# Performance work log

Measured on AMD Instinct MI355X. Metric: run time of the kernel, lower is better.

Reference implementation:

```python
import jax, jax.numpy as jnp
import numpy as np

B_GRAPHS = 64
N_PER = 8192
N = B_GRAPHS * N_PER          # 524288 nodes
E = N * 24                    # 12582912 edges
F0 = 8                        # num_node_features
FE = 4                        # num_edge_features
HID = 5                       # embedding_size, heads=1
ACT = 4                       # num_actions
GOAL = 6                      # goal_size
EPS = 1e-5


def _graph_norm(x, batch, w, b, ms):
    # PyG GraphNorm: per-graph mean/var with learnable mean_scale
    cnt = jax.ops.segment_sum(jnp.ones((x.shape[0],), x.dtype), batch, num_segments=B_GRAPHS)[:, None]
    mean = jax.ops.segment_sum(x, batch, num_segments=B_GRAPHS) / cnt
    sub = x - ms * mean[batch]
    var = jax.ops.segment_sum(sub * sub, batch, num_segments=B_GRAPHS) / cnt
    return w * sub * jax.lax.rsqrt(var[batch] + EPS) + b


def _gatv2(x, edge_index, edge_attr, Wl, bl, Wr, br, We, att, bo):
    # GATv2Conv, heads=1, add_self_loops=True (self-loop edge_attr = mean of edge_attr)
    n = x.shape[0]
    loop = jnp.arange(n, dtype=edge_index.dtype)
    src = jnp.concatenate([edge_index[0], loop])
    dst = jnp.concatenate([edge_index[1], loop])
    ea = jnp.concatenate([edge_attr, jnp.broadcast_to(edge_attr.mean(0), (n, edge_attr.shape[1]))], axis=0)
    xl = x @ Wl + bl            # source transform [n, HID]
    xr = x @ Wr + br            # target transform [n, HID]
    xl_src = xl[src]            # [E+n, HID]
    e = jax.nn.leaky_relu(xl_src + xr[dst] + ea @ We, 0.2)
    logits = e @ att            # [E+n]
    m = jax.ops.segment_max(logits, dst, num_segments=n)
    ex = jnp.exp(logits - m[dst])
    alpha = ex / jax.ops.segment_sum(ex, dst, num_segments=n)[dst]
    return jax.ops.segment_sum(alpha[:, None] * xl_src, dst, num_segments=n) + bo


def reference(x, edge_index, edge_attr, batch, current_node_ids, action_mask, one_hot_goal,
              gn_w, gn_b, gn_ms,
              Wl1, bl1, Wr1, br1, We1, att1, bo1,
              Wl2, bl2, Wr2, br2, We2, att2, bo2,
              Wv1, bv1, Wv2, bv2, Wa1, ba1, Wa2, ba2):
    x = _graph_norm(x, batch, gn_w, gn_b, gn_ms)
    identity = x
    h = jax.nn.relu(_gatv2(x, edge_index, edge_attr, Wl1, bl1, Wr1, br1, We1, att1, bo1))
    x = jnp.concatenate([h, identity], axis=1)    # [N, 13]
    identity = x
    h = jax.nn.relu(_gatv2(x, edge_index, edge_attr, Wl2, bl2, Wr2, br2, We2, att2, bo2))
    x = jnp.concatenate([h, identity], axis=1)    # [N, 18]
    cnt = jnp.bincount(batch, length=B_GRAPHS)
    pool = jax.ops.segment_sum(x, batch, num_segments=B_GRAPHS) / cnt[:, None].astype(x.dtype)
    offsets = jnp.concatenate([jnp.zeros((1,), cnt.dtype), jnp.cumsum(cnt)[:-1]])
    xg = x[current_node_ids + offsets]            # [B, 18]
    feat = jnp.concatenate([xg, pool, one_hot_goal], axis=1)  # [B, 42]
    adv = jax.nn.relu(feat @ Wa1 + ba1) @ Wa2 + ba2
    val = jax.nn.relu(feat @ Wv1 + bv1) @ Wv2 + bv2
    q = val + adv - adv.mean(axis=1, keepdims=True)
    return jnp.where(action_mask == 0, jnp.asarray(-1e8, q.dtype), q)


def setup_inputs():
    key = jax.random.key(0)
    k = jax.random.split(key, 24)
    lin_w = lambda kk, i, o: (jax.random.normal(kk, (i, o), jnp.float32) / np.sqrt(i)).astype(jnp.float32)
    x = jax.random.normal(k[0], (N, F0), jnp.float32)
    g = jax.random.randint(k[1], (E,), 0, B_GRAPHS)
    src = g * N_PER + jax.random.randint(k[2], (E,), 0, N_PER)
    dst = g * N_PER + jax.random.randint(k[3], (E,), 0, N_PER)
    edge_index = jnp.stack([src, dst]).astype(jnp.int32)
    edge_attr = jax.random.normal(k[4], (E, FE), jnp.float32)
    batch = (jnp.arange(N) // N_PER).astype(jnp.int32)
    current_node_ids = jax.random.randint(k[5], (B_GRAPHS,), 0, N_PER).astype(jnp.int32)
    action_mask = jax.random.randint(k[6], (B_GRAPHS, ACT), 0, 2).astype(jnp.int32)
    one_hot_goal = jax.nn.one_hot(jax.random.randint(k[7], (B_GRAPHS,), 0, GOAL), GOAL, dtype=jnp.float32)
    inp = dict(x=x, edge_index=edge_index, edge_attr=edge_attr, batch=batch,
               current_node_ids=current_node_ids, action_mask=action_mask, one_hot_goal=one_hot_goal)
    inp.update(gn_w=jnp.ones((F0,)), gn_b=jnp.zeros((F0,)), gn_ms=jnp.ones((F0,)))
    inp.update(Wl1=lin_w(k[8], F0, HID), bl1=jnp.zeros((HID,)), Wr1=lin_w(k[9], F0, HID), br1=jnp.zeros((HID,)),
               We1=lin_w(k[10], FE, HID), att1=jax.random.normal(k[11], (HID,), jnp.float32), bo1=jnp.zeros((HID,)))
    inp.update(Wl2=lin_w(k[12], 13, HID), bl2=jnp.zeros((HID,)), Wr2=lin_w(k[13], 13, HID), br2=jnp.zeros((HID,)),
               We2=lin_w(k[14], FE, HID), att2=jax.random.normal(k[15], (HID,), jnp.float32), bo2=jnp.zeros((HID,)))
    inp.update(Wv1=lin_w(k[16], 42, 10), bv1=jnp.zeros((10,)), Wv2=lin_w(k[17], 10, 1), bv2=jnp.zeros((1,)),
               Wa1=lin_w(k[18], 42, 10), ba1=jnp.zeros((10,)), Wa2=lin_w(k[19], 10, ACT), ba2=jnp.zeros((ACT,)))
    return inp
```

## Files before the change

### kernel.cpp

```cpp
#include <hip/hip_runtime.h>
#include <hip/hip_bf16.h>
#include <stdint.h>

#define NG   64
#define NPER 8192
#define NN   (NG * NPER)
#define NE   (NN * 24)
#define F0   8

#define NBIN   1024
#define BROWS  512
#define BCAP   13312
#define SCHUNK 8192
#define NBLK   (NE / SCHUNK)

__device__ __forceinline__ void atomAddF(float* p, float v) {
    unsafeAtomicAdd(p, v);
}

__device__ __forceinline__ uint32_t pk_bf16(float a, float b) {
    return (__float_as_uint(a) >> 16) | (__float_as_uint(b) & 0xFFFF0000u);
}
__device__ __forceinline__ float lo_bf16(uint32_t u) { return __uint_as_float(u << 16); }
__device__ __forceinline__ float hi_bf16(uint32_t u) { return __uint_as_float(u & 0xFFFF0000u); }

__global__ void k_stats(const float* __restrict__ x, float* __restrict__ stats) {
    int b = blockIdx.x;
    int g = b >> 2;
    int seg = b & 3;
    int t = threadIdx.x;
    float sum[8] = {0,0,0,0,0,0,0,0};
    float sq[8]  = {0,0,0,0,0,0,0,0};
    int base = g * NPER + seg * 2048;
    for (int r = t; r < 2048; r += 256) {
        const float4* row = (const float4*)(x + (size_t)(base + r) * F0);
        float4 ra = row[0], rb = row[1];
        float v0=ra.x,v1=ra.y,v2=ra.z,v3=ra.w,v4=rb.x,v5=rb.y,v6=rb.z,v7=rb.w;
        sum[0]+=v0; sq[0]+=v0*v0; sum[1]+=v1; sq[1]+=v1*v1;
        sum[2]+=v2; sq[2]+=v2*v2; sum[3]+=v3; sq[3]+=v3*v3;
        sum[4]+=v4; sq[4]+=v4*v4; sum[5]+=v5; sq[5]+=v5*v5;
        sum[6]+=v6; sq[6]+=v6*v6; sum[7]+=v7; sq[7]+=v7*v7;
    }
    #pragma unroll
    for (int f = 0; f < 8; f++) {
        float s = sum[f], q = sq[f];
        for (int off = 32; off > 0; off >>= 1) {
            s += __shfl_down(s, off);
            q += __shfl_down(q, off);
        }
        if ((t & 63) == 0) {
            atomAddF(stats + g*16 + f, s);
            atomAddF(stats + g*16 + 8 + f, q);
        }
    }
}

__global__ void k_norm(const float* __restrict__ x, const float* __restrict__ stats,
                       const float* __restrict__ gw, const float* __restrict__ gb,
                       const float* __restrict__ gms,
                       const float* __restrict__ Wl, const float* __restrict__ bl,
                       const float* __restrict__ Wr, const float* __restrict__ br,
                       float* __restrict__ xn, uint4* __restrict__ xlc,
                       float* __restrict__ xr1) {
    int g = blockIdx.x >> 5;
    int n = blockIdx.x * 256 + threadIdx.x;
    const float invc = 1.0f / (float)NPER;
    float xnf[8];
    const float4* row4 = (const float4*)(x + (size_t)n * F0);
    float4 ra = row4[0], rb = row4[1];
    float rv[8] = {ra.x, ra.y, ra.z, ra.w, rb.x, rb.y, rb.z, rb.w};
    #pragma unroll
    for (int f = 0; f < 8; f++) {
        float m   = stats[g*16 + f] * invc;
        float ex2 = stats[g*16 + 8 + f] * invc;
        float ms  = gms[f];
        float var = ex2 - 2.0f*ms*m*m + ms*ms*m*m;
        float sub = rv[f] - ms * m;
        xnf[f] = gw[f] * sub * rsqrtf(var + 1e-5f) + gb[f];
    }
    float4* xnr = (float4*)(xn + (size_t)n * 8);
    xnr[0] = make_float4(xnf[0], xnf[1], xnf[2], xnf[3]);
    xnr[1] = make_float4(xnf[4], xnf[5], xnf[6], xnf[7]);
    float xlv[5], xrv[5];
    #pragma unroll
    for (int j = 0; j < 5; j++) {
        float a = bl[j], b = br[j];
        #pragma unroll
        for (int f = 0; f < 8; f++) { a += xnf[f] * Wl[f*5 + j]; b += xnf[f] * Wr[f*5 + j]; }
        xlv[j] = a; xrv[j] = b;
    }
    uint4 p;
    p.x = pk_bf16(xlv[0], xlv[1]);
    p.y = pk_bf16(xlv[2], xlv[3]);
    p.z = pk_bf16(xlv[4], 0.0f);
    p.w = 0u;
    xlc[n] = p;
    float4* xrr = (float4*)(xr1 + (size_t)n * 8);
    xrr[0] = make_float4(xrv[0], xrv[1], xrv[2], xrv[3]);
    xrr[1] = make_float4(xrv[4], 0.f, 0.f, 0.f);
}

__global__ __launch_bounds__(1024) void k_bin(
        const int* __restrict__ src, const int* __restrict__ dst,
        const float4* __restrict__ eattr,
        unsigned* __restrict__ gfill, uint2* __restrict__ payload,
        float* __restrict__ easum) {
    __shared__ unsigned lc[NBIN];
    __shared__ unsigned lstart[NBIN];
    __shared__ unsigned lalloc[NBIN];
    __shared__ unsigned lbase[NBIN];
    __shared__ uint2 stage[SCHUNK];
    __shared__ float ls[16][4];
    __shared__ unsigned wsum[16];
    int t = threadIdx.x;
    int lane = t & 63, wv = t >> 6;
    int base = blockIdx.x * SCHUNK;
    lc[t] = 0u;
    __syncthreads();
    int dc[SCHUNK/1024];
    #pragma unroll
    for (int k = 0; k < SCHUNK/1024; k++) dc[k] = dst[base + k*1024 + t];
    #pragma unroll
    for (int k = 0; k < SCHUNK/1024; k++)
        atomicAdd(&lc[((unsigned)dc[k]) >> 9], 1u);
    __syncthreads();
    unsigned c = lc[t];
    unsigned s = c;
    #pragma unroll
    for (int d = 1; d < 64; d <<= 1) {
        unsigned u = (unsigned)__shfl_up((int)s, d);
        if (lane >= d) s += u;
    }
    if (lane == 63) wsum[wv] = s;
    __syncthreads();
    if (t < 16) {
        unsigned v = wsum[t], sv = v;
        #pragma unroll
        for (int d = 1; d < 16; d <<= 1) {
            unsigned u = (unsigned)__shfl_up((int)sv, d);
            if (t >= d) sv += u;
        }
        wsum[t] = sv - v;
    }
    __syncthreads();
    unsigned excl = s + wsum[wv] - c;
    lstart[t] = excl;
    lalloc[t] = excl;
    lbase[t]  = c ? atomicAdd(&gfill[t], c) : 0u;
    __syncthreads();
    float e0 = 0.f, e1 = 0.f, e2 = 0.f, e3 = 0.f;
    unsigned xwv[SCHUNK/1024], ywv[SCHUNK/1024], bv[SCHUNK/1024], pos[SCHUNK/1024];
    #pragma unroll
    for (int k = 0; k < SCHUNK/1024; k++) {
        int e = base + k*1024 + t;
        int sv2 = src[e];
        int d = dc[k];
        float4 ea = eattr[e];
        e0 += ea.x; e1 += ea.y; e2 += ea.z; e3 += ea.w;
        bv[k] = ((unsigned)d) >> 9;
        xwv[k] = (unsigned)(sv2 & 8191) | ((unsigned)(d & 511) << 13) | (bv[k] << 22);
        ywv[k] = __builtin_amdgcn_cvt_pk_fp8_f32(ea.z, ea.w,
                    __builtin_amdgcn_cvt_pk_fp8_f32(ea.x, ea.y, 0, false), true);
    }
    #pragma unroll
    for (int k = 0; k < SCHUNK/1024; k++) pos[k] = atomicAdd(&lalloc[bv[k]], 1u);
    #pragma unroll
    for (int k = 0; k < SCHUNK/1024; k++) stage[pos[k]] = make_uint2(xwv[k], ywv[k]);
    __syncthreads();
    for (int i = t; i < SCHUNK; i += 1024) {
        uint2 r = stage[i];
        unsigned b = r.x >> 22;
        unsigned loc = lbase[b] + ((unsigned)i - lstart[b]);
        if (loc < BCAP) payload[(size_t)b * BCAP + loc] = r;
    }
    for (int off = 32; off > 0; off >>= 1) {
        e0 += __shfl_down(e0, off); e1 += __shfl_down(e1, off);
        e2 += __shfl_down(e2, off); e3 += __shfl_down(e3, off);
    }
    if ((t & 63) == 0) { ls[wv][0]=e0; ls[wv][1]=e1; ls[wv][2]=e2; ls[wv][3]=e3; }
    __syncthreads();
    if (t < 4) {
        float v = 0.f;
        #pragma unroll
        for (int k = 0; k < 16; k++) v += ls[k][t];
        atomAddF(easum + t, v);
    }
}

template<int PASS>
__global__ __launch_bounds__(1024) void k_edge(
        const uint2* __restrict__ payload, const unsigned* __restrict__ gfill,
        const uint4* __restrict__ xlcv, const float* __restrict__ xrf,
        const float* __restrict__ xn, const float* __restrict__ h1in,
        const float* __restrict__ We, const float* __restrict__ att,
        const float* __restrict__ bo, const float* __restrict__ easum,
        const float* __restrict__ Wl2, const float* __restrict__ bl2,
        const float* __restrict__ Wr2, const float* __restrict__ br2,
        float* __restrict__ h1out, uint4* __restrict__ xl2c, float* __restrict__ xr2,
        const int* __restrict__ cur, float* __restrict__ pool, float* __restrict__ xg) {
    __shared__ uint2 stage[BCAP + 6];
    __shared__ unsigned cnt_s[BROWS];
    __shared__ unsigned scan_s[BROWS];
    __shared__ unsigned alloc_s[BROWS];
    __shared__ unsigned wscan[8];
    __shared__ float lsum[16][18];
    int t = threadIdx.x;
    int lane = t & 63, wvi = t >> 6;
    int bin = ((blockIdx.x & 7) << 7) + (blockIdx.x >> 3);
    int g = bin >> 4;

    unsigned CNT = gfill[bin];
    if (CNT > BCAP) CNT = BCAP;
    const uint2* pA = payload + (size_t)bin * BCAP;

    uint2 rcv[13];
    #pragma unroll
    for (int k = 0; k < 13; ++k) {
        unsigned idx = (unsigned)(k * 1024) + (unsigned)t;
        rcv[k] = (idx < CNT) ? pA[idx] : make_uint2(0u, 0u);
    }
    if (t < BROWS) cnt_s[t] = 0u;
    __syncthreads();
    #pragma unroll
    for (int k = 0; k < 13; ++k) {
        unsigned idx = (unsigned)(k * 1024) + (unsigned)t;
        if (idx < CNT) atomicAdd(&cnt_s[(rcv[k].x >> 13) & 511u], 1u);
    }
    __syncthreads();
    unsigned c = 0, s = 0;
    if (t < BROWS) {
        c = cnt_s[t];
        s = c;
        #pragma unroll
        for (int d = 1; d < 64; d <<= 1) {
            unsigned u = (unsigned)__shfl_up((int)s, d);
            if (lane >= d) s += u;
        }
        if (lane == 63) wscan[wvi] = s;
    }
    __syncthreads();
    if (t < 8) {
        unsigned v = wscan[t], sv = v;
        #pragma unroll
        for (int d = 1; d < 8; d <<= 1) {
            unsigned u = (unsigned)__shfl_up((int)sv, d);
            if (t >= d) sv += u;
        }
        wscan[t] = sv - v;
    }
    __syncthreads();
    if (t < BROWS) {
        unsigned incl = s + wscan[wvi];
        scan_s[t]  = incl;
        alloc_s[t] = incl - c;
    }
    __syncthreads();
    unsigned pos[13];
    #pragma unroll
    for (int k = 0; k < 13; ++k) {
        unsigned idx = (unsigned)(k * 1024) + (unsigned)t;
        pos[k] = (idx < CNT) ? atomicAdd(&alloc_s[(rcv[k].x >> 13) & 511u], 1u) : 0u;
    }
    #pragma unroll
    for (int k = 0; k < 13; ++k) {
        unsigned idx = (unsigned)(k * 1024) + (unsigned)t;
        if (idx < CNT) stage[pos[k]] = rcv[k];
    }
    __syncthreads();

    int r = t >> 1, sub = t & 1;
    int n = (bin << 9) + r;
    unsigned end   = scan_s[r];
    unsigned start = end - cnt_s[r];

    float w0[5], w1[5], w2[5], w3[5], av[5];
    #pragma unroll
    for (int j = 0; j < 5; j++) {
        w0[j] = We[j]; w1[j] = We[5+j]; w2[j] = We[10+j]; w3[j] = We[15+j];
        av[j] = att[j];
    }
    const uint4* xlg = xlcv + ((size_t)g << 13);
    const float4* xr4 = (const float4*)(xrf + (size_t)n * 8);
    float4 q0 = xr4[0], q1 = xr4[1];
    float xrv[5] = {q0.x, q0.y, q0.z, q0.w, q1.x};

    float acc[5] = {0.f, 0.f, 0.f, 0.f, 0.f};
    float aw = 0.f;

    unsigned i0 = start + (unsigned)sub;
    uint2 r0 = stage[i0];
    uint4 x0 = xlg[r0.x & 8191u];
    uint2 r1 = stage[i0 + 2];
    uint4 x1 = xlg[r1.x & 8191u];
    for (unsigned i = i0; i < end; i += 2) {
        uint2 rn = stage[i + 4];
        uint4 xf = xlg[rn.x & 8191u];
        float xs[5] = {lo_bf16(x0.x), hi_bf16(x0.x),
                       lo_bf16(x0.y), hi_bf16(x0.y), lo_bf16(x0.z)};
        float eax = __builtin_amdgcn_cvt_f32_fp8(r0.y, 0);
        float eay = __builtin_amdgcn_cvt_f32_fp8(r0.y, 1);
        float eaz = __builtin_amdgcn_cvt_f32_fp8(r0.y, 2);
        float eaw = __builtin_amdgcn_cvt_f32_fp8(r0.y, 3);
        float lg = 0.f;
        #pragma unroll
        for (int j = 0; j < 5; j++) {
            float z = xs[j] + xrv[j] + w0[j]*eax + w1[j]*eay + w2[j]*eaz + w3[j]*eaw;
            z = z > 0.f ? z : 0.2f * z;
            lg += z * av[j];
        }
        float w = __expf(lg);
        aw += w;
        #pragma unroll
        for (int j = 0; j < 5; j++) acc[j] += w * xs[j];
        r0 = r1; x0 = x1; r1 = rn; x1 = xf;
    }
    aw += __shfl_xor(aw, 1);
    #pragma unroll
    for (int j = 0; j < 5; j++) acc[j] += __shfl_xor(acc[j], 1);

    const float invE = 1.0f / (float)NE;
    float eaM[5];
    #pragma unroll
    for (int j = 0; j < 5; j++)
        eaM[j] = (easum[0]*w0[j] + easum[1]*w1[j] + easum[2]*w2[j] + easum[3]*w3[j]) * invE;
    uint4 xw = xlcv[n];
    float xlv[5] = {lo_bf16(xw.x), hi_bf16(xw.x),
                    lo_bf16(xw.y), hi_bf16(xw.y), lo_bf16(xw.z)};
    float lg = 0.f;
    #pragma unroll
    for (int j = 0; j < 5; j++) {
        float z = xlv[j] + xrv[j] + eaM[j];
        z = z > 0.f ? z : 0.2f * z;
        lg += z * av[j];
    }
    float wsl = __expf(lg);
    float den = aw + wsl;
    float h[5];
    #pragma unroll
    for (int j = 0; j < 5; j++) {
        float v = (acc[j] + wsl * xlv[j]) / den + bo[j];
        h[j] = v > 0.f ? v : 0.f;
    }
    const float4* xnr = (const float4*)(xn + (size_t)n * 8);
    float4 xa = xnr[0], xb = xnr[1];

    if (PASS == 1) {
        float x2[13];
        #pragma unroll
        for (int j = 0; j < 5; j++) x2[j] = h[j];
        x2[5] = xa.x; x2[6] = xa.y; x2[7] = xa.z; x2[8] = xa.w;
        x2[9] = xb.x; x2[10] = xb.y; x2[11] = xb.z; x2[12] = xb.w;
        const float* Wx = sub ? Wr2 : Wl2;
        const float* bx = sub ? br2 : bl2;
        float o[5];
        #pragma unroll
        for (int j = 0; j < 5; j++) {
            float a = bx[j];
            #pragma unroll
            for (int k = 0; k < 13; k++) a += x2[k] * Wx[k*5 + j];
            o[j] = a;
        }
        if (sub) {
            float4* xr2r = (float4*)(xr2 + (size_t)n * 8);
            xr2r[0] = make_float4(o[0], o[1], o[2], o[3]);
            xr2r[1] = make_float4(o[4], 0.f, 0.f, 0.f);
            float4* h1r = (float4*)(h1out + (size_t)n * 8);
            h1r[0] = make_float4(h[0], h[1], h[2], h[3]);
            (h1out + (size_t)n * 8)[4] = h[4];
        } else {
            uint4 p;
            p.x = pk_bf16(o[0], o[1]);
            p.y = pk_bf16(o[2], o[3]);
            p.z = pk_bf16(o[4], 0.0f);
            p.w = 0u;
            xl2c[n] = p;
        }
    } else {
        float x3[18];
        #pragma unroll
        for (int j = 0; j < 5; j++) x3[j] = h[j];
        const float* h1r = h1in + (size_t)n * 8;
        #pragma unroll
        for (int j = 0; j < 5; j++) x3[5 + j] = h1r[j];
        x3[10] = xa.x; x3[11] = xa.y; x3[12] = xa.z; x3[13] = xa.w;
        x3[14] = xb.x; x3[15] = xb.y; x3[16] = xb.z; x3[17] = xb.w;
        #pragma unroll
        for (int f = 0; f < 18; f++) {
            float v = sub ? 0.f : x3[f];
            for (int off = 32; off > 0; off >>= 1) v += __shfl_down(v, off);
            if ((t & 63) == 0) lsum[wvi][f] = v;
        }
        __syncthreads();
        if (t < 18) {
            float v = 0.f;
            #pragma unroll
            for (int k = 0; k < 16; k++) v += lsum[k][t];
            atomAddF(pool + g*18 + t, v);
        }
        if (!sub && ((n & (NPER - 1)) == cur[g])) {
            #pragma unroll
            for (int f = 0; f < 18; f++) xg[g*18 + f] = x3[f];
        }
    }
}

__global__ void k_head(const float* __restrict__ xg, const float* __restrict__ pool,
                       const float* __restrict__ goal, const int* __restrict__ am,
                       const float* __restrict__ Wv1, const float* __restrict__ bv1,
                       const float* __restrict__ Wv2, const float* __restrict__ bv2,
                       const float* __restrict__ Wa1, const float* __restrict__ ba1,
                       const float* __restrict__ Wa2, const float* __restrict__ ba2,
                       float* __restrict__ out) {
    int g = threadIdx.x;
    if (g >= NG) return;
    float feat[42];
    #pragma unroll
    for (int f = 0; f < 18; f++) feat[f] = xg[g*18 + f];
    #pragma unroll
    for (int f = 0; f < 18; f++) feat[18 + f] = pool[g*18 + f] * (1.0f / (float)NPER);
    #pragma unroll
    for (int f = 0; f < 6; f++) feat[36 + f] = goal[g*6 + f];
    float hv[10], ha[10];
    #pragma unroll
    for (int j = 0; j < 10; j++) {
        float a = bv1[j], b = ba1[j];
        for (int k = 0; k < 42; k++) { a += feat[k] * Wv1[k*10 + j]; b += feat[k] * Wa1[k*10 + j]; }
        hv[j] = a > 0.f ? a : 0.f;
        ha[j] = b > 0.f ? b : 0.f;
    }
    float val = bv2[0];
    #pragma unroll
    for (int k = 0; k < 10; k++) val += hv[k] * Wv2[k];
    float adv[4];
    #pragma unroll
    for (int a2 = 0; a2 < 4; a2++) {
        float s = ba2[a2];
        #pragma unroll
        for (int k = 0; k < 10; k++) s += ha[k] * Wa2[k*4 + a2];
        adv[a2] = s;
    }
    float mean = 0.25f * (adv[0] + adv[1] + adv[2] + adv[3]);
    #pragma unroll
    for (int a2 = 0; a2 < 4; a2++) {
        float q = val + adv[a2] - mean;
        if (am[g*4 + a2] == 0) q = -1e8f;
        out[g*4 + a2] = q;
    }
}

extern "C" void kernel_launch(void* const* d_in, const int* in_sizes, int n_in,
                              void* d_out, int out_size, void* d_ws, size_t ws_size,
                              hipStream_t stream) {
    const float* x     = (const float*)d_in[0];
    const int*   ei    = (const int*)  d_in[1];
    const float* eattr = (const float*)d_in[2];
    const int*   cur   = (const int*)  d_in[4];
    const int*   am    = (const int*)  d_in[5];
    const float* goal  = (const float*)d_in[6];
    const float* gw    = (const float*)d_in[7];
    const float* gb    = (const float*)d_in[8];
    const float* gms   = (const float*)d_in[9];
    const float* Wl1   = (const float*)d_in[10];
    const float* bl1   = (const float*)d_in[11];
    const float* Wr1   = (const float*)d_in[12];
    const float* br1   = (const float*)d_in[13];
    const float* We1   = (const float*)d_in[14];
    const float* att1  = (const float*)d_in[15];
    const float* bo1   = (const float*)d_in[16];
    const float* Wl2   = (const float*)d_in[17];
    const float* bl2   = (const float*)d_in[18];
    const float* Wr2   = (const float*)d_in[19];
    const float* br2   = (const float*)d_in[20];
    const float* We2   = (const float*)d_in[21];
    const float* att2  = (const float*)d_in[22];
    const float* bo2   = (const float*)d_in[23];
    const float* Wv1   = (const float*)d_in[24];
    const float* bv1   = (const float*)d_in[25];
    const float* Wv2   = (const float*)d_in[26];
    const float* bv2   = (const float*)d_in[27];
    const float* Wa1   = (const float*)d_in[28];
    const float* ba1   = (const float*)d_in[29];
    const float* Wa2   = (const float*)d_in[30];
    const float* ba2   = (const float*)d_in[31];

    float* ws   = (float*)d_ws;
    float* xn   = ws;
    float* xr1  = xn  + (size_t)NN * 8;
    float* xr2  = xr1 + (size_t)NN * 8;
    float* h1   = xr2 + (size_t)NN * 8;
    uint4* xlc  = (uint4*)(h1 + (size_t)NN * 8);
    uint4* xl2c = xlc + (size_t)NN;
    uint2* payload = (uint2*)(xl2c + (size_t)NN);
    unsigned* gfill = (unsigned*)(payload + (size_t)NBIN * BCAP + 8);
    float* stats = (float*)(gfill + NBIN);
    float* easum = stats + NG * 16;
    float* pool  = easum + 4;
    float* xg    = pool + NG * 18;

    size_t zbytes = (size_t)(NBIN + NG*16 + 4 + NG*18) * 4;
    hipMemsetAsync(gfill, 0, zbytes, stream);

    k_stats<<<256, 256, 0, stream>>>(x, stats);
    k_norm<<<NN/256, 256, 0, stream>>>(x, stats, gw, gb, gms, Wl1, bl1, Wr1, br1,
                                       xn, xlc, xr1);
    k_bin<<<NBLK, 1024, 0, stream>>>(ei, ei + NE, (const float4*)eattr,
                                     gfill, payload, easum);
    k_edge<1><<<NBIN, 1024, 0, stream>>>(payload, gfill, xlc, xr1, xn, nullptr,
                                         We1, att1, bo1, easum,
                                         Wl2, bl2, Wr2, br2,
                                         h1, xl2c, xr2,
                                         nullptr, nullptr, nullptr);
    k_edge<2><<<NBIN, 1024, 0, stream>>>(payload, gfill, xl2c, xr2, xn, h1,
                                         We2, att2, bo2, easum,
                                         nullptr, nullptr, nullptr, nullptr,
                                         nullptr, nullptr, nullptr,
                                         cur, pool, xg);
    k_head<<<1, 64, 0, stream>>>(xg, pool, goal, am, Wv1, bv1, Wv2, bv2,
                                 Wa1, ba1, Wa2, ba2, (float*)d_out);
}
```

Measured before the change: 681.2 us.

## Process edge bins in two LDS halves to raise occupancy

```diff
diff --git a/kernel.cpp b/kernel.cpp
--- a/kernel.cpp
+++ b/kernel.cpp
@@ -11,6 +11,7 @@
 #define NBIN   1024
 #define BROWS  512
 #define BCAP   13312
+#define SHALF  6656
 #define SCHUNK 8192
 #define NBLK   (NE / SCHUNK)
 
@@ -100,15 +101,13 @@
     xrr[1] = make_float4(xrv[4], 0.f, 0.f, 0.f);
 }
 
-__global__ __launch_bounds__(1024) void k_bin(
+__global__ __launch_bounds__(1024, 8) void k_bin(
         const int* __restrict__ src, const int* __restrict__ dst,
         const float4* __restrict__ eattr,
         unsigned* __restrict__ gfill, uint2* __restrict__ payload,
         float* __restrict__ easum) {
     __shared__ unsigned lc[NBIN];
-    __shared__ unsigned lstart[NBIN];
-    __shared__ unsigned lalloc[NBIN];
-    __shared__ unsigned lbase[NBIN];
+    __shared__ unsigned diff[NBIN];
     __shared__ uint2 stage[SCHUNK];
     __shared__ float ls[16][4];
     __shared__ unsigned wsum[16];
@@ -144,9 +143,9 @@
     }
     __syncthreads();
     unsigned excl = s + wsum[wv] - c;
-    lstart[t] = excl;
-    lalloc[t] = excl;
-    lbase[t]  = c ? atomicAdd(&gfill[t], c) : 0u;
+    unsigned gbase = c ? atomicAdd(&gfill[t], c) : 0u;
+    lc[t]   = excl;
+    diff[t] = gbase - excl;
     __syncthreads();
     float e0 = 0.f, e1 = 0.f, e2 = 0.f, e3 = 0.f;
     unsigned xwv[SCHUNK/1024], ywv[SCHUNK/1024], bv[SCHUNK/1024], pos[SCHUNK/1024];
@@ -163,14 +162,14 @@
                     __builtin_amdgcn_cvt_pk_fp8_f32(ea.x, ea.y, 0, false), true);
     }
     #pragma unroll
-    for (int k = 0; k < SCHUNK/1024; k++) pos[k] = atomicAdd(&lalloc[bv[k]], 1u);
+    for (int k = 0; k < SCHUNK/1024; k++) pos[k] = atomicAdd(&lc[bv[k]], 1u);
     #pragma unroll
     for (int k = 0; k < SCHUNK/1024; k++) stage[pos[k]] = make_uint2(xwv[k], ywv[k]);
     __syncthreads();
     for (int i = t; i < SCHUNK; i += 1024) {
         uint2 r = stage[i];
         unsigned b = r.x >> 22;
-        unsigned loc = lbase[b] + ((unsigned)i - lstart[b]);
+        unsigned loc = (unsigned)i + diff[b];
         if (loc < BCAP) payload[(size_t)b * BCAP + loc] = r;
     }
     for (int off = 32; off > 0; off >>= 1) {
@@ -188,7 +187,7 @@
 }
 
 template<int PASS>
-__global__ __launch_bounds__(1024) void k_edge(
+__global__ __launch_bounds__(1024, 8) void k_edge(
         const uint2* __restrict__ payload, const unsigned* __restrict__ gfill,
         const uint4* __restrict__ xlcv, const float* __restrict__ xrf,
         const float* __restrict__ xn, const float* __restrict__ h1in,
@@ -198,7 +197,7 @@
         const float* __restrict__ Wr2, const float* __restrict__ br2,
         float* __restrict__ h1out, uint4* __restrict__ xl2c, float* __restrict__ xr2,
         const int* __restrict__ cur, float* __restrict__ pool, float* __restrict__ xg) {
-    __shared__ uint2 stage[BCAP + 6];
+    __shared__ uint2 stage[SHALF + 8];
     __shared__ unsigned cnt_s[BROWS];
     __shared__ unsigned scan_s[BROWS];
     __shared__ unsigned alloc_s[BROWS];
@@ -213,72 +212,14 @@
     if (CNT > BCAP) CNT = BCAP;
     const uint2* pA = payload + (size_t)bin * BCAP;
 
-    uint2 rcv[13];
-    #pragma unroll
-    for (int k = 0; k < 13; ++k) {
-        unsigned idx = (unsigned)(k * 1024) + (unsigned)t;
-        rcv[k] = (idx < CNT) ? pA[idx] : make_uint2(0u, 0u);
-    }
-    if (t < BROWS) cnt_s[t] = 0u;
-    __syncthreads();
-    #pragma unroll
-    for (int k = 0; k < 13; ++k) {
-        unsigned idx = (unsigned)(k * 1024) + (unsigned)t;
-        if (idx < CNT) atomicAdd(&cnt_s[(rcv[k].x >> 13) & 511u], 1u);
-    }
-    __syncthreads();
-    unsigned c = 0, s = 0;
-    if (t < BROWS) {
-        c = cnt_s[t];
-        s = c;
-        #pragma unroll
-        for (int d = 1; d < 64; d <<= 1) {
-            unsigned u = (unsigned)__shfl_up((int)s, d);
-            if (lane >= d) s += u;
-        }
-        if (lane == 63) wscan[wvi] = s;
-    }
-    __syncthreads();
-    if (t < 8) {
-        unsigned v = wscan[t], sv = v;
-        #pragma unroll
-        for (int d = 1; d < 8; d <<= 1) {
-            unsigned u = (unsigned)__shfl_up((int)sv, d);
-            if (t >= d) sv += u;
-        }
-        wscan[t] = sv - v;
-    }
-    __syncthreads();
-    if (t < BROWS) {
-        unsigned incl = s + wscan[wvi];
-        scan_s[t]  = incl;
-        alloc_s[t] = incl - c;
-    }
-    __syncthreads();
-    unsigned pos[13];
-    #pragma unroll
-    for (int k = 0; k < 13; ++k) {
-        unsigned idx = (unsigned)(k * 1024) + (unsigned)t;
-        pos[k] = (idx < CNT) ? atomicAdd(&alloc_s[(rcv[k].x >> 13) & 511u], 1u) : 0u;
-    }
-    #pragma unroll
-    for (int k = 0; k < 13; ++k) {
-        unsigned idx = (unsigned)(k * 1024) + (unsigned)t;
-        if (idx < CNT) stage[pos[k]] = rcv[k];
-    }
-    __syncthreads();
-
-    int r = t >> 1, sub = t & 1;
-    int n = (bin << 9) + r;
-    unsigned end   = scan_s[r];
-    unsigned start = end - cnt_s[r];
-
     float w0[5], w1[5], w2[5], w3[5], av[5];
     #pragma unroll
     for (int j = 0; j < 5; j++) {
         w0[j] = We[j]; w1[j] = We[5+j]; w2[j] = We[10+j]; w3[j] = We[15+j];
         av[j] = att[j];
     }
+    int r = t >> 1, sub = t & 1;
+    int n = (bin << 9) + r;
     const uint4* xlg = xlcv + ((size_t)g << 13);
     const float4* xr4 = (const float4*)(xrf + (size_t)n * 8);
     float4 q0 = xr4[0], q1 = xr4[1];
@@ -287,32 +228,95 @@
     float acc[5] = {0.f, 0.f, 0.f, 0.f, 0.f};
     float aw = 0.f;
 
-    unsigned i0 = start + (unsigned)sub;
-    uint2 r0 = stage[i0];
-    uint4 x0 = xlg[r0.x & 8191u];
-    uint2 r1 = stage[i0 + 2];
-    uint4 x1 = xlg[r1.x & 8191u];
-    for (unsigned i = i0; i < end; i += 2) {
-        uint2 rn = stage[i + 4];
-        uint4 xf = xlg[rn.x & 8191u];
-        float xs[5] = {lo_bf16(x0.x), hi_bf16(x0.x),
-                       lo_bf16(x0.y), hi_bf16(x0.y), lo_bf16(x0.z)};
-        float eax = __builtin_amdgcn_cvt_f32_fp8(r0.y, 0);
-        float eay = __builtin_amdgcn_cvt_f32_fp8(r0.y, 1);
-        float eaz = __builtin_amdgcn_cvt_f32_fp8(r0.y, 2);
-        float eaw = __builtin_amdgcn_cvt_f32_fp8(r0.y, 3);
-        float lg = 0.f;
-        #pragma unroll
-        for (int j = 0; j < 5; j++) {
-            float z = xs[j] + xrv[j] + w0[j]*eax + w1[j]*eay + w2[j]*eaz + w3[j]*eaw;
-            z = z > 0.f ? z : 0.2f * z;
-            lg += z * av[j];
-        }
-        float w = __expf(lg);
-        aw += w;
-        #pragma unroll
-        for (int j = 0; j < 5; j++) acc[j] += w * xs[j];
-        r0 = r1; x0 = x1; r1 = rn; x1 = xf;
+    #pragma unroll
+    for (int hh = 0; hh < 2; ++hh) {
+        unsigned b0 = (unsigned)hh * SHALF;
+        unsigned ch = (CNT > b0) ? (CNT - b0) : 0u;
+        if (ch > SHALF) ch = SHALF;
+        uint2 rcv[7];
+        #pragma unroll
+        for (int k = 0; k < 7; ++k) {
+            unsigned idx = (unsigned)(k * 1024) + (unsigned)t;
+            rcv[k] = (idx < ch) ? pA[b0 + idx] : make_uint2(0u, 0u);
+        }
+        if (t < BROWS) cnt_s[t] = 0u;
+        __syncthreads();
+        #pragma unroll
+        for (int k = 0; k < 7; ++k) {
+            unsigned idx = (unsigned)(k * 1024) + (unsigned)t;
+            if (idx < ch) atomicAdd(&cnt_s[(rcv[k].x >> 13) & 511u], 1u);
+        }
+        __syncthreads();
+        unsigned c = 0, s = 0;
+        if (t < BROWS) {
+            c = cnt_s[t];
+            s = c;
+            #pragma unroll
+            for (int d = 1; d < 64; d <<= 1) {
+                unsigned u = (unsigned)__shfl_up((int)s, d);
+                if (lane >= d) s += u;
+            }
+            if (lane == 63) wscan[wvi] = s;
+        }
+        __syncthreads();
+        if (t < 8) {
+            unsigned v = wscan[t], sv = v;
+            #pragma unroll
+            for (int d = 1; d < 8; d <<= 1) {
+                unsigned u = (unsigned)__shfl_up((int)sv, d);
+                if (t >= d) sv += u;
+            }
+            wscan[t] = sv - v;
+        }
+        __syncthreads();
+        if (t < BROWS) {
+            unsigned incl = s + wscan[wvi];
+            scan_s[t]  = incl;
+            alloc_s[t] = incl - c;
+        }
+        __syncthreads();
+        unsigned pos[7];
+        #pragma unroll
+        for (int k = 0; k < 7; ++k) {
+            unsigned idx = (unsigned)(k * 1024) + (unsigned)t;
+            pos[k] = (idx < ch) ? atomicAdd(&alloc_s[(rcv[k].x >> 13) & 511u], 1u) : 0u;
+        }
+        #pragma unroll
+        for (int k = 0; k < 7; ++k) {
+            unsigned idx = (unsigned)(k * 1024) + (unsigned)t;
+            if (idx < ch) stage[pos[k]] = rcv[k];
+        }
+        __syncthreads();
+        unsigned end   = scan_s[r];
+        unsigned start = end - cnt_s[r];
+        unsigned i0 = start + (unsigned)sub;
+        uint2 r0 = stage[i0];
+        uint4 x0 = xlg[r0.x & 8191u];
+        uint2 r1 = stage[i0 + 2];
+        uint4 x1 = xlg[r1.x & 8191u];
+        for (unsigned i = i0; i < end; i += 2) {
+            uint2 rn = stage[i + 4];
+            uint4 xf = xlg[rn.x & 8191u];
+            float xs[5] = {lo_bf16(x0.x), hi_bf16(x0.x),
+                           lo_bf16(x0.y), hi_bf16(x0.y), lo_bf16(x0.z)};
+            float eax = __builtin_amdgcn_cvt_f32_fp8(r0.y, 0);
+            float eay = __builtin_amdgcn_cvt_f32_fp8(r0.y, 1);
+            float eaz = __builtin_amdgcn_cvt_f32_fp8(r0.y, 2);
+            float eaw = __builtin_amdgcn_cvt_f32_fp8(r0.y, 3);
+            float lg = 0.f;
+            #pragma unroll
+            for (int j = 0; j < 5; j++) {
+                float z = xs[j] + xrv[j] + w0[j]*eax + w1[j]*eay + w2[j]*eaz + w3[j]*eaw;
+                z = z > 0.f ? z : 0.2f * z;
+                lg += z * av[j];
+            }
+            float w = __expf(lg);
+            aw += w;
+            #pragma unroll
+            for (int j = 0; j < 5; j++) acc[j] += w * xs[j];
+            r0 = r1; x0 = x1; r1 = rn; x1 = xf;
+        }
+        __syncthreads();
     }
     aw += __shfl_xor(aw, 1);
     #pragma unroll
```

Measured after the change: 669.7 us. Within noise of the previous version (-1.7%).
